# Kernel tuning notes

Measured on AMD Instinct MI355X. Metric: run time of the kernel, lower is better.

## Reference

```python
import jax, jax.numpy as jnp
import numpy as np

B, S, H, I, RH, P, K, NH = 4, 1024, 1024, 4096, 256, 16, 4, 16
TEMP = 1.0


def setup_inputs() -> dict:
    key = jax.random.key(0)
    ks = jax.random.split(key, 10)
    g = lambda k, shape: (jax.random.normal(k, shape, jnp.float32) * 0.02)
    return {
        "hidden_states": jax.random.normal(ks[0], (B, S, H), jnp.float32),
        "ln1_w": jnp.ones((H,), jnp.float32),
        "ln1_b": jnp.zeros((H,), jnp.float32),
        "Wqkv": g(ks[1], (3 * H, H)),
        "bqkv": jnp.zeros((3 * H,), jnp.float32),
        "Wo": g(ks[2], (H, H)),
        "bo": jnp.zeros((H,), jnp.float32),
        "ln2_w": jnp.ones((H,), jnp.float32),
        "ln2_b": jnp.zeros((H,), jnp.float32),
        "Wr1": g(ks[3], (RH, H)),
        "br1": jnp.zeros((RH,), jnp.float32),
        "Wr2": g(ks[4], (P, RH)),
        "br2": jnp.zeros((P,), jnp.float32),
        "W1": g(ks[5], (I, H)),
        "b1": jnp.zeros((I,), jnp.float32),
        "W2": g(ks[6], (H, I)),
        "b2": jnp.zeros((H,), jnp.float32),
    }


def _layernorm(x, w, b, eps=1e-5):
    m = x.mean(-1, keepdims=True)
    v = jnp.mean((x - m) ** 2, axis=-1, keepdims=True)
    return (x - m) * jax.lax.rsqrt(v + eps) * w + b


def _forward(hidden_states, ln1_w, ln1_b, Wqkv, bqkv, Wo, bo,
             ln2_w, ln2_b, Wr1, br1, Wr2, br2, W1, b1, W2, b2):
    Dh = H // NH
    # --- attention sub-block (GPT-2 style causal self-attention) ---
    x = _layernorm(hidden_states, ln1_w, ln1_b)
    qkv = x @ Wqkv.T + bqkv                                  # [B,S,3H]
    q, k, v = jnp.split(qkv, 3, axis=-1)
    split = lambda t: t.reshape(B, S, NH, Dh).transpose(0, 2, 1, 3)  # [B,NH,S,Dh]
    q, k, v = split(q), split(k), split(v)
    scores = jnp.einsum('bhqd,bhkd->bhqk', q, k) * (1.0 / np.float32(np.sqrt(Dh)))
    causal = jnp.tril(jnp.ones((S, S), bool))
    scores = jnp.where(causal, scores, jnp.float32(-1e9))
    attn = jax.nn.softmax(scores, axis=-1)
    ctx = jnp.einsum('bhqk,bhkd->bhqd', attn, v)
    ctx = ctx.transpose(0, 2, 1, 3).reshape(B, S, H)
    h = hidden_states + ctx @ Wo.T + bo                      # residual 1

    # --- routed MLP sub-block ---
    x2 = _layernorm(h, ln2_w, ln2_b)
    # router MLP (eval mode: no dropout)
    r = jax.nn.relu(x2 @ Wr1.T + br1) @ Wr2.T + br2          # [B,S,P]
    probs = jax.nn.softmax(r / TEMP, axis=-1)
    top_vals, top_idx = jax.lax.top_k(probs, K)              # [B,S,K]
    # scatter top-k probs back to pathway axis, then renormalize
    sel = jnp.sum(jax.nn.one_hot(top_idx, P, dtype=probs.dtype) * top_vals[..., None], axis=-2)  # [B,S,P]
    w = sel / (sel.sum(-1, keepdims=True) + 1e-8)

    # block-diagonal pathway MLP: pathway p uses contiguous slices of W1/W2
    Hp, Ip = H // P, I // P
    pidx = jnp.arange(P)
    W1b = W1.reshape(P, Ip, P, Hp)[pidx, :, pidx, :]         # [P,Ip,Hp]
    b1b = b1.reshape(P, Ip)
    W2b = W2.reshape(P, Hp, P, Ip)[pidx, :, pidx, :]         # [P,Hp,Ip]
    b2b = b2.reshape(P, Hp)
    hb = x2.reshape(B, S, P, Hp)
    inter = jax.nn.gelu(jnp.einsum('bsph,pih->bspi', hb, W1b) + b1b)
    po = jnp.einsum('bspi,phi->bsph', inter, W2b) + b2b       # [B,S,P,Hp]
    mlp_out = (po * w[..., None]).reshape(B, S, H)
    return h + mlp_out


def reference(hidden_states, ln1_w, ln1_b, Wqkv, bqkv, Wo, bo,
              ln2_w, ln2_b, Wr1, br1, Wr2, br2, W1, b1, W2, b2):
    return _forward(hidden_states, ln1_w, ln1_b, Wqkv, bqkv, Wo, bo,
                    ln2_w, ln2_b, Wr1, br1, Wr2, br2, W1, b1, W2, b2)
```

## Files before the change

kernel.cpp:

```cpp
#include <hip/hip_runtime.h>


#define USH unsigned short

typedef __attribute__((ext_vector_type(8))) short s16x8;
typedef __attribute__((ext_vector_type(4))) float f32x4;

__device__ __forceinline__ float bf2f(USH u) {
    union { unsigned int i; float f; } x; x.i = ((unsigned int)u) << 16; return x.f;
}
__device__ __forceinline__ USH f2bf(float f) {
    unsigned int x = __float_as_uint(f);
    unsigned int r = (x + 0x7fffu + ((x >> 16) & 1u)) >> 16;
    return (USH)r;
}
__device__ __forceinline__ const USH* pick(const void* raw, const USH* ar, bool bf16in) {
    return bf16in ? (const USH*)raw : ar;
}

__device__ __forceinline__ void async16(const USH* g, USH* lds_base) {
    __builtin_amdgcn_global_load_lds((const __attribute__((address_space(1))) unsigned int*)g,
                                     (__attribute__((address_space(3))) unsigned int*)lds_base,
                                     16, 0, 0);
}

struct CvtArgs {
    const void* src[17];
    unsigned off[18];
};

__global__ __launch_bounds__(256) void convert_kernel(CvtArgs a, USH* __restrict__ arena,
                                                      const unsigned* __restrict__ det)
{
    if (*det != 0x3F800000u) return;
    int s = blockIdx.y + 1;
    unsigned n4 = (a.off[s + 1] - a.off[s]) >> 2;
    ushort4* dst = (ushort4*)(arena + a.off[s]);
    const float4* sf = (const float4*)a.src[s];
    for (unsigned i = blockIdx.x * 256u + threadIdx.x; i < n4; i += gridDim.x * 256u) {
        float4 f = sf[i];
        ushort4 o;
        o.x = f2bf(f.x); o.y = f2bf(f.y); o.z = f2bf(f.z); o.w = f2bf(f.w);
        dst[i] = o;
    }
}

__global__ __launch_bounds__(256) void ln_kernel(const void* __restrict__ in,
                                                 const unsigned* __restrict__ det,
                                                 const void* __restrict__ gwr, const USH* __restrict__ gwa,
                                                 const void* __restrict__ gbr, const USH* __restrict__ gba,
                                                 const unsigned* __restrict__ wdet,
                                                 USH* __restrict__ out)
{
    bool bf16w = (*wdet != 0x3F800000u);
    const USH* gw = pick(gwr, gwa, bf16w);
    const USH* gb = pick(gbr, gba, bf16w);
    int row = blockIdx.x, tid = threadIdx.x;
    bool bf16in = det && (*det != 0x3F800000u);
    float v0, v1, v2, v3;
    if (bf16in) {
        const USH* r = (const USH*)in + (size_t)row * 1024 + tid * 4;
        ushort4 u = *(const ushort4*)r;
        v0 = bf2f(u.x); v1 = bf2f(u.y); v2 = bf2f(u.z); v3 = bf2f(u.w);
    } else {
        const float* r = (const float*)in + (size_t)row * 1024 + tid * 4;
        float4 f = *(const float4*)r;
        v0 = f.x; v1 = f.y; v2 = f.z; v3 = f.w;
    }
    float s = v0 + v1 + v2 + v3;
    float q = v0*v0 + v1*v1 + v2*v2 + v3*v3;
    #pragma unroll
    for (int o = 32; o >= 1; o >>= 1) { s += __shfl_xor(s, o); q += __shfl_xor(q, o); }
    __shared__ float rs[4], rq[4];
    int wid = tid >> 6;
    if ((tid & 63) == 0) { rs[wid] = s; rq[wid] = q; }
    __syncthreads();
    float S = rs[0] + rs[1] + rs[2] + rs[3];
    float Q = rq[0] + rq[1] + rq[2] + rq[3];
    float mean = S * (1.0f / 1024.0f);
    float var  = Q * (1.0f / 1024.0f) - mean * mean;
    float rstd = rsqrtf(var + 1e-5f);
    int c = tid * 4;
    ushort4 wv = *(const ushort4*)(gw + c);
    ushort4 bv = *(const ushort4*)(gb + c);
    ushort4 o4;
    o4.x = f2bf((v0 - mean) * rstd * bf2f(wv.x) + bf2f(bv.x));
    o4.y = f2bf((v1 - mean) * rstd * bf2f(wv.y) + bf2f(bv.y));
    o4.z = f2bf((v2 - mean) * rstd * bf2f(wv.z) + bf2f(bv.z));
    o4.w = f2bf((v3 - mean) * rstd * bf2f(wv.w) + bf2f(bv.w));
    *(ushort4*)(out + (size_t)row * 1024 + c) = o4;
}

template<int RT, int CT>
__global__ __launch_bounds__(256) void gemm_t(
    const USH* __restrict__ A,
    const void* __restrict__ Wraw, const USH* __restrict__ Warena,
    const void* __restrict__ braw, const USH* __restrict__ barena,
    void* __restrict__ Cout, const void* __restrict__ resid,
    int M, int N, int K, int mode, const unsigned* __restrict__ det)
{
    constexpr int BM = 32 * RT, BN = 32 * CT;
    constexpr int NA8 = BM / 8, NC8 = (BM + BN) / 8, NPW = NC8 / 4;
    bool bf16in = (*det != 0x3F800000u);
    const USH* W    = pick(Wraw, Warena, bf16in);
    const USH* bias = pick(braw, barena, bf16in);
    __shared__ __align__(16) USH As[BM * 64];
    __shared__ __align__(16) USH Bs[BN * 64];
    int tid = threadIdx.x;
    int w = tid >> 6, lane = tid & 63, l15 = lane & 15, quad = lane >> 4;
    int wm = (w & 1) * 16 * RT, wn = (w >> 1) * 16 * CT;
    int m0 = blockIdx.x * BM, n0 = blockIdx.y * BN;
    int lr8 = lane >> 3, g = (lane & 7) ^ lr8;
    int sw = l15 & 7;

    const USH* cp[NPW]; USH* lp[NPW];
    #pragma unroll
    for (int i = 0; i < NPW; ++i) {
        int c = w + 4 * i;
        if (c < NA8) { cp[i] = A + (size_t)(m0 + c * 8 + lr8) * K + g * 8;            lp[i] = &As[c * 512]; }
        else         { cp[i] = W + (size_t)(n0 + (c - NA8) * 8 + lr8) * K + g * 8;    lp[i] = &Bs[(c - NA8) * 512]; }
    }
    f32x4 acc[RT][CT] = {};
    for (int k0 = 0; k0 < K; k0 += 64) {
        __syncthreads();
        #pragma unroll
        for (int i = 0; i < NPW; ++i) { async16(cp[i], lp[i]); cp[i] += 64; }
        __syncthreads();
        s16x8 af[RT][2], bfr[CT][2];
        #pragma unroll
        for (int i = 0; i < RT; ++i) {
            int r = wm + 16*i + l15;
            af[i][0] = *(const s16x8*)&As[r * 64 + ((quad       ^ sw) * 8)];
            af[i][1] = *(const s16x8*)&As[r * 64 + (((quad + 4) ^ sw) * 8)];
        }
        #pragma unroll
        for (int j = 0; j < CT; ++j) {
            int r = wn + 16*j + l15;
            bfr[j][0] = *(const s16x8*)&Bs[r * 64 + ((quad       ^ sw) * 8)];
            bfr[j][1] = *(const s16x8*)&Bs[r * 64 + (((quad + 4) ^ sw) * 8)];
        }
        #pragma unroll
        for (int i = 0; i < RT; ++i)
            #pragma unroll
            for (int j = 0; j < CT; ++j) {
                acc[i][j] = __builtin_amdgcn_mfma_f32_16x16x32_bf16(af[i][0], bfr[j][0], acc[i][j], 0, 0, 0);
                acc[i][j] = __builtin_amdgcn_mfma_f32_16x16x32_bf16(af[i][1], bfr[j][1], acc[i][j], 0, 0, 0);
            }
    }
    bool rf32 = !bf16in;
    float bv[CT];
    #pragma unroll
    for (int j = 0; j < CT; ++j) bv[j] = bf2f(bias[n0 + wn + 16*j + l15]);
    #pragma unroll
    for (int i = 0; i < RT; ++i) {
        int mrow = m0 + wm + 16*i + quad * 4;
        #pragma unroll
        for (int j = 0; j < CT; ++j) {
            int n = n0 + wn + 16*j + l15;
            #pragma unroll
            for (int r = 0; r < 4; ++r) {
                int m = mrow + r;
                float val = acc[i][j][r] + bv[j];
                if (mode == 3) val = fmaxf(val, 0.0f);
                if (mode == 2) {
                    size_t idx = (size_t)m * N + n;
                    val += rf32 ? ((const float*)resid)[idx] : bf2f(((const USH*)resid)[idx]);
                }
                if (mode == 1) {
                    int which = n >> 10, head = (n >> 6) & 15, d = n & 63;
                    int b = m >> 10, sdx = m & 1023;
                    ((USH*)Cout)[(((size_t)(which * 64 + b * 16 + head)) * 1024 + sdx) * 64 + d] = f2bf(val);
                } else {
                    ((float*)Cout)[(size_t)m * N + n] = val;
                }
            }
        }
    }
}

__global__ __launch_bounds__(256) void attn_mfma(const USH* __restrict__ qkv,
                                                 USH* __restrict__ ctx)
{
    int bh = blockIdx.x;
    int qb = (gridDim.y - 1) - blockIdx.y;
    int q0 = qb * 64;
    int tid = threadIdx.x, w = tid >> 6, lane = tid & 63, l15 = lane & 15, quad = lane >> 4;
    __shared__ __align__(16) USH Kt[64][72];
    __shared__ __align__(16) USH Vt[80][72];
    __shared__ __align__(16) USH Pb[4][16][72];
    const USH* Qb = qkv + (size_t)bh * 65536;
    const USH* Kb = qkv + (size_t)(64 + bh) * 65536;
    const USH* Vb = qkv + (size_t)(128 + bh) * 65536;
    s16x8 qf[2];
    {
        const USH* qp = Qb + (size_t)(q0 + 16*w + l15) * 64 + quad * 8;
        qf[0] = *(const s16x8*)qp;
        qf[1] = *(const s16x8*)(qp + 32);
    }
    for (int i = tid; i < 16 * 72; i += 256) (&Vt[64][0])[i] = 0x3F80;
    f32x4 oacc[4] = {};
    f32x4 lacc = {};
    int sr = tid & 63, scb = tid >> 6;
    int rowb = 16*w + quad * 4;
    for (int kt = 0; kt <= qb; ++kt) {
        int k0 = kt << 6;
        __syncthreads();
        {
            const USH* kg = Kb + (size_t)(k0 + sr) * 64 + scb * 16;
            uint4 k0v = *(const uint4*)kg;
            uint4 k1v = *(const uint4*)(kg + 8);
            *(uint4*)&Kt[sr][scb * 16]     = k0v;
            *(uint4*)&Kt[sr][scb * 16 + 8] = k1v;
            const USH* vg = Vb + (size_t)(k0 + sr) * 64 + scb * 16;
            uint4 v0v = *(const uint4*)vg;
            uint4 v1v = *(const uint4*)(vg + 8);
            USH tmp[16];
            *(uint4*)tmp       = v0v;
            *(uint4*)(tmp + 8) = v1v;
            #pragma unroll
            for (int i = 0; i < 16; ++i) Vt[scb * 16 + i][sr] = tmp[i];
        }
        __syncthreads();
        f32x4 sacc[4] = {};
        #pragma unroll
        for (int t = 0; t < 4; ++t) {
            s16x8 kf0 = *(const s16x8*)&Kt[16*t + l15][quad * 8];
            s16x8 kf1 = *(const s16x8*)&Kt[16*t + l15][32 + quad * 8];
            sacc[t] = __builtin_amdgcn_mfma_f32_16x16x32_bf16(qf[0], kf0, sacc[t], 0, 0, 0);
            sacc[t] = __builtin_amdgcn_mfma_f32_16x16x32_bf16(qf[1], kf1, sacc[t], 0, 0, 0);
        }
        bool diag = (kt == qb);
        #pragma unroll
        for (int t = 0; t < 4; ++t)
            #pragma unroll
            for (int r = 0; r < 4; ++r) {
                bool masked = diag && (16*t + l15 > rowb + r);
                float pv = masked ? 0.0f : __expf(sacc[t][r] * 0.125f);
                Pb[w][quad*4 + r][16*t + l15] = f2bf(pv);
            }
        s16x8 pf0 = *(const s16x8*)&Pb[w][l15][quad * 8];
        s16x8 pf1 = *(const s16x8*)&Pb[w][l15][32 + quad * 8];
        #pragma unroll
        for (int t = 0; t < 4; ++t) {
            s16x8 vf0 = *(const s16x8*)&Vt[16*t + l15][quad * 8];
            s16x8 vf1 = *(const s16x8*)&Vt[16*t + l15][32 + quad * 8];
            oacc[t] = __builtin_amdgcn_mfma_f32_16x16x32_bf16(pf0, vf0, oacc[t], 0, 0, 0);
            oacc[t] = __builtin_amdgcn_mfma_f32_16x16x32_bf16(pf1, vf1, oacc[t], 0, 0, 0);
        }
        s16x8 of0 = *(const s16x8*)&Vt[64 + l15][quad * 8];
        s16x8 of1 = *(const s16x8*)&Vt[64 + l15][32 + quad * 8];
        lacc = __builtin_amdgcn_mfma_f32_16x16x32_bf16(pf0, of0, lacc, 0, 0, 0);
        lacc = __builtin_amdgcn_mfma_f32_16x16x32_bf16(pf1, of1, lacc, 0, 0, 0);
    }
    int b = bh >> 4, hh = bh & 15;
    float inv[4];
    #pragma unroll
    for (int r = 0; r < 4; ++r) inv[r] = 1.0f / lacc[r];
    #pragma unroll
    for (int t = 0; t < 4; ++t)
        #pragma unroll
        for (int r = 0; r < 4; ++r) {
            int q = q0 + 16*w + quad * 4 + r;
            int d = 16*t + l15;
            ctx[((size_t)(b * 1024 + q)) * 1024 + hh * 64 + d] = f2bf(oacc[t][r] * inv[r]);
        }
}

__global__ __launch_bounds__(64) void router_kernel(const float* __restrict__ r1,
                                                    const void* __restrict__ Wr2raw, const USH* __restrict__ Wr2a,
                                                    const void* __restrict__ br2raw, const USH* __restrict__ br2a,
                                                    const unsigned* __restrict__ det,
                                                    float* __restrict__ wout)
{
    bool bf16in = (*det != 0x3F800000u);
    const USH* Wr2 = pick(Wr2raw, Wr2a, bf16in);
    const USH* br2 = pick(br2raw, br2a, bf16in);
    int tok = blockIdx.x, lane = threadIdx.x;
    int p = lane & 15, c = lane >> 4;
    const float* row = r1 + (size_t)tok * 256;
    const USH* wr = Wr2 + p * 256 + c * 64;
    float s = 0.0f;
    #pragma unroll
    for (int i = 0; i < 64; i += 4) {
        ushort4 u = *(const ushort4*)(wr + i);
        s = fmaf(bf2f(u.x), row[c*64 + i + 0], s);
        s = fmaf(bf2f(u.y), row[c*64 + i + 1], s);
        s = fmaf(bf2f(u.z), row[c*64 + i + 2], s);
        s = fmaf(bf2f(u.w), row[c*64 + i + 3], s);
    }
    s += __shfl_xor(s, 16);
    s += __shfl_xor(s, 32);
    s += bf2f(br2[p]);
    float mx = s;
    #pragma unroll
    for (int o = 8; o >= 1; o >>= 1) mx = fmaxf(mx, __shfl_xor(mx, o));
    float e = __expf(s - mx);
    float sum = e;
    #pragma unroll
    for (int o = 8; o >= 1; o >>= 1) sum += __shfl_xor(sum, o);
    float prob = e / sum;
    int rank = 0;
    int base = lane & 48;
    #pragma unroll
    for (int j = 0; j < 16; ++j) {
        float pj = __shfl(prob, base + j);
        rank += (pj > prob) || (pj == prob && j < p);
    }
    float sel = (rank < 4) ? prob : 0.0f;
    float ssum = sel;
    #pragma unroll
    for (int o = 8; o >= 1; o >>= 1) ssum += __shfl_xor(ssum, o);
    float wv = sel / (ssum + 1e-8f);
    if (lane < 16) wout[(size_t)tok * 16 + lane] = wv;
}

__global__ __launch_bounds__(256) void pw1_kernel(
    const USH* __restrict__ x2,
    const void* __restrict__ W1raw, const USH* __restrict__ W1a,
    const void* __restrict__ b1raw, const USH* __restrict__ b1a,
    USH* __restrict__ inter, const unsigned* __restrict__ det)
{
    bool bf16in = (*det != 0x3F800000u);
    const USH* W1 = pick(W1raw, W1a, bf16in);
    const USH* b1 = pick(b1raw, b1a, bf16in);
    int p = blockIdx.z;
    __shared__ __align__(16) USH As[64 * 64];
    __shared__ __align__(16) USH Bs[128 * 64];
    int tid = threadIdx.x;
    int w = tid >> 6, lane = tid & 63, l15 = lane & 15, quad = lane >> 4;
    int wm = (w & 1) * 32, wn = (w >> 1) * 64;
    int m0 = blockIdx.x * 64, n0 = blockIdx.y * 128;
    int lr8 = lane >> 3, g = (lane & 7) ^ lr8;
    int sw = l15 & 7;

    #pragma unroll
    for (int i = 0; i < 6; ++i) {
        int c = w + 4 * i;
        if (c < 8) async16(x2 + (size_t)(m0 + c * 8 + lr8) * 1024 + p * 64 + g * 8, &As[c * 512]);
        else       async16(W1 + (size_t)(p * 256 + n0 + (c - 8) * 8 + lr8) * 1024 + p * 64 + g * 8, &Bs[(c - 8) * 512]);
    }
    __syncthreads();
    f32x4 acc[2][4] = {};
    s16x8 af[2][2], bfr[4][2];
    #pragma unroll
    for (int i = 0; i < 2; ++i) {
        int r = wm + 16*i + l15;
        af[i][0] = *(const s16x8*)&As[r * 64 + ((quad       ^ sw) * 8)];
        af[i][1] = *(const s16x8*)&As[r * 64 + (((quad + 4) ^ sw) * 8)];
    }
    #pragma unroll
    for (int j = 0; j < 4; ++j) {
        int r = wn + 16*j + l15;
        bfr[j][0] = *(const s16x8*)&Bs[r * 64 + ((quad       ^ sw) * 8)];
        bfr[j][1] = *(const s16x8*)&Bs[r * 64 + (((quad + 4) ^ sw) * 8)];
    }
    #pragma unroll
    for (int i = 0; i < 2; ++i)
        #pragma unroll
        for (int j = 0; j < 4; ++j) {
            acc[i][j] = __builtin_amdgcn_mfma_f32_16x16x32_bf16(af[i][0], bfr[j][0], acc[i][j], 0, 0, 0);
            acc[i][j] = __builtin_amdgcn_mfma_f32_16x16x32_bf16(af[i][1], bfr[j][1], acc[i][j], 0, 0, 0);
        }
    #pragma unroll
    for (int j = 0; j < 4; ++j) {
        int n = n0 + wn + 16*j + l15;
        float bias1 = bf2f(b1[p * 256 + n]);
        #pragma unroll
        for (int i = 0; i < 2; ++i) {
            int mrow = m0 + wm + 16*i + quad * 4;
            #pragma unroll
            for (int r = 0; r < 4; ++r) {
                float s = acc[i][j][r] + bias1;
                float u = 0.7978845608028654f * (s + 0.044715f * s * s * s);
                float e = __expf(2.0f * u);
                float gl = s * (1.0f - 1.0f / (e + 1.0f));
                inter[((size_t)p * 4096 + mrow + r) * 256 + n] = f2bf(gl);
            }
        }
    }
}

__global__ __launch_bounds__(256) void pw2_kernel(
    const USH* __restrict__ inter, const float* __restrict__ hbuf,
    const float* __restrict__ wbuf,
    const void* __restrict__ W2raw, const USH* __restrict__ W2a,
    const void* __restrict__ b2raw, const USH* __restrict__ b2a,
    void* __restrict__ out, const unsigned* __restrict__ det)
{
    bool bf16in = (*det != 0x3F800000u);
    const USH* W2 = pick(W2raw, W2a, bf16in);
    const USH* b2 = pick(b2raw, b2a, bf16in);
    int p = blockIdx.y;
    __shared__ __align__(16) USH As[64 * 64];
    __shared__ __align__(16) USH Bs[64 * 64];
    int tid = threadIdx.x;
    int w = tid >> 6, lane = tid & 63, l15 = lane & 15, quad = lane >> 4;
    int wm = (w & 1) * 32, wn = (w >> 1) * 32;
    int m0 = blockIdx.x * 64;
    int lr8 = lane >> 3, g = (lane & 7) ^ lr8;
    int sw = l15 & 7;

    const USH* cp[4]; USH* lp[4];
    #pragma unroll
    for (int i = 0; i < 4; ++i) {
        int c = w + 4 * i;
        if (c < 8) { cp[i] = inter + ((size_t)p * 4096 + m0 + c * 8 + lr8) * 256 + g * 8; lp[i] = &As[c * 512]; }
        else       { cp[i] = W2 + (size_t)(p * 64 + (c - 8) * 8 + lr8) * 4096 + p * 256 + g * 8; lp[i] = &Bs[(c - 8) * 512]; }
    }
    f32x4 acc[2][2] = {};
    #pragma unroll
    for (int ks = 0; ks < 4; ++ks) {
        __syncthreads();
        #pragma unroll
        for (int i = 0; i < 4; ++i) { async16(cp[i], lp[i]); cp[i] += 64; }
        __syncthreads();
        s16x8 af[2][2], bfr[2][2];
        #pragma unroll
        for (int i = 0; i < 2; ++i) {
            int r = wm + 16*i + l15;
            af[i][0] = *(const s16x8*)&As[r * 64 + ((quad       ^ sw) * 8)];
            af[i][1] = *(const s16x8*)&As[r * 64 + (((quad + 4) ^ sw) * 8)];
        }
        #pragma unroll
        for (int j = 0; j < 2; ++j) {
            int r = wn + 16*j + l15;
            bfr[j][0] = *(const s16x8*)&Bs[r * 64 + ((quad       ^ sw) * 8)];
            bfr[j][1] = *(const s16x8*)&Bs[r * 64 + (((quad + 4) ^ sw) * 8)];
        }
        #pragma unroll
        for (int i = 0; i < 2; ++i)
            #pragma unroll
            for (int j = 0; j < 2; ++j) {
                acc[i][j] = __builtin_amdgcn_mfma_f32_16x16x32_bf16(af[i][0], bfr[j][0], acc[i][j], 0, 0, 0);
                acc[i][j] = __builtin_amdgcn_mfma_f32_16x16x32_bf16(af[i][1], bfr[j][1], acc[i][j], 0, 0, 0);
            }
    }
    bool f32out = !bf16in;
    #pragma unroll
    for (int i = 0; i < 2; ++i) {
        int tok0 = m0 + wm + 16*i + quad * 4;
        float wp[4];
        #pragma unroll
        for (int r = 0; r < 4; ++r) wp[r] = wbuf[(size_t)(tok0 + r) * 16 + p];
        #pragma unroll
        for (int j = 0; j < 2; ++j) {
            int hl = wn + 16*j + l15;
            int hcol = p * 64 + hl;
            float bias2 = bf2f(b2[p * 64 + hl]);
            #pragma unroll
            for (int r = 0; r < 4; ++r) {
                size_t o = (size_t)(tok0 + r) * 1024 + hcol;
                float val = hbuf[o] + (acc[i][j][r] + bias2) * wp[r];
                if (f32out) ((float*)out)[o] = val;
                else        ((USH*)out)[o]   = f2bf(val);
            }
        }
    }
}

extern "C" void kernel_launch(void* const* d_in, const int* in_sizes, int n_in,
                              void* d_out, int out_size, void* d_ws, size_t ws_size,
                              hipStream_t stream) {
    (void)n_in; (void)out_size; (void)ws_size;
    const unsigned* det = (const unsigned*)d_in[1];

    CvtArgs ca;
    unsigned off = 0;
    for (int i = 0; i < 17; ++i) { ca.src[i] = d_in[i]; ca.off[i] = off; off += (unsigned)in_sizes[i]; }
    ca.off[17] = off;

    USH* arena = (USH*)d_ws;
    const USH* ln1w_a = arena + ca.off[1];
    const USH* ln1b_a = arena + ca.off[2];
    const USH* Wqkv_a = arena + ca.off[3];
    const USH* bqkv_a = arena + ca.off[4];
    const USH* Wo_a   = arena + ca.off[5];
    const USH* bo_a   = arena + ca.off[6];
    const USH* ln2w_a = arena + ca.off[7];
    const USH* ln2b_a = arena + ca.off[8];
    const USH* Wr1_a  = arena + ca.off[9];
    const USH* br1_a  = arena + ca.off[10];
    const USH* Wr2_a  = arena + ca.off[11];
    const USH* br2_a  = arena + ca.off[12];
    const USH* W1_a   = arena + ca.off[13];
    const USH* b1_a   = arena + ca.off[14];
    const USH* W2_a   = arena + ca.off[15];
    const USH* b2_a   = arena + ca.off[16];

    size_t arenaB = ((size_t)off * 2 + 255) & ~(size_t)255;
    char* base = (char*)d_ws;
    USH*   x     = (USH*)(base + arenaB);
    USH*   qkvt  = (USH*)(base + arenaB + 8388608);
    float* h     = (float*)(base + arenaB + 8388608 + 25165824);
    USH*   x2    = (USH*)(base + arenaB + 8388608 + 25165824 + 16777216);
    float* r1    = (float*)qkvt;
    float* wbuf  = (float*)(base + arenaB + 8388608 + 25165824 + 16777216 + 8388608);
    USH*   inter = x;
    USH*   ctx   = x;

    convert_kernel<<<dim3(256, 16), 256, 0, stream>>>(ca, arena, det);
    ln_kernel<<<4096, 256, 0, stream>>>(d_in[0], det, d_in[1], ln1w_a, d_in[2], ln1b_a, det, x);
    gemm_t<4,4><<<dim3(32, 24), 256, 0, stream>>>(x, d_in[3], Wqkv_a, d_in[4], bqkv_a, qkvt, nullptr, 4096, 3072, 1024, 1, det);
    attn_mfma<<<dim3(64, 16), 256, 0, stream>>>(qkvt, ctx);
    gemm_t<4,4><<<dim3(32, 8), 256, 0, stream>>>(ctx, d_in[5], Wo_a, d_in[6], bo_a, h, d_in[0], 4096, 1024, 1024, 2, det);
    ln_kernel<<<4096, 256, 0, stream>>>(h, nullptr, d_in[7], ln2w_a, d_in[8], ln2b_a, det, x2);
    gemm_t<2,2><<<dim3(64, 4), 256, 0, stream>>>(x2, d_in[9], Wr1_a, d_in[10], br1_a, r1, nullptr, 4096, 256, 1024, 3, det);
    router_kernel<<<4096, 64, 0, stream>>>(r1, d_in[11], Wr2_a, d_in[12], br2_a, det, wbuf);
    pw1_kernel<<<dim3(64, 2, 16), 256, 0, stream>>>(x2, d_in[13], W1_a, d_in[14], b1_a, inter, det);
    pw2_kernel<<<dim3(64, 16), 256, 0, stream>>>(inter, h, wbuf, d_in[15], W2_a, d_in[16], b2_a, d_out, det);
}
```

Baseline: 298.7 us.

## Fuse pathway MLP up/down projections into one kernel and shrink GEMM tiles

Merges the two pathway MLP kernels into a single kernel. Each block computes the GELU intermediate for 64 tokens and all 256 intermediate columns and keeps it in LDS (64KB, swizzled), then runs the down-projection from LDS. This removes the global write and read of the bf16 intermediate and one launch, but uses more LDS per block and more accumulator registers, which may reduce occupancy. The Wo and router GEMMs also switch to smaller tile templates with larger grids, to get more blocks onto the CUs.

Measured after the change: 285.0 us. 1.05x faster.

```diff
diff --git a/kernel.cpp b/kernel.cpp
--- a/kernel.cpp
+++ b/kernel.cpp
@@ -314,143 +314,136 @@
     if (lane < 16) wout[(size_t)tok * 16 + lane] = wv;
 }
 
-__global__ __launch_bounds__(256) void pw1_kernel(
+__global__ __launch_bounds__(256) void pw_fused(
     const USH* __restrict__ x2,
     const void* __restrict__ W1raw, const USH* __restrict__ W1a,
     const void* __restrict__ b1raw, const USH* __restrict__ b1a,
-    USH* __restrict__ inter, const unsigned* __restrict__ det)
+    const void* __restrict__ W2raw, const USH* __restrict__ W2a,
+    const void* __restrict__ b2raw, const USH* __restrict__ b2a,
+    const float* __restrict__ hbuf, const float* __restrict__ wbuf,
+    void* __restrict__ out, const unsigned* __restrict__ det)
 {
     bool bf16in = (*det != 0x3F800000u);
     const USH* W1 = pick(W1raw, W1a, bf16in);
     const USH* b1 = pick(b1raw, b1a, bf16in);
-    int p = blockIdx.z;
-    __shared__ __align__(16) USH As[64 * 64];
-    __shared__ __align__(16) USH Bs[128 * 64];
-    int tid = threadIdx.x;
-    int w = tid >> 6, lane = tid & 63, l15 = lane & 15, quad = lane >> 4;
-    int wm = (w & 1) * 32, wn = (w >> 1) * 64;
-    int m0 = blockIdx.x * 64, n0 = blockIdx.y * 128;
-    int lr8 = lane >> 3, g = (lane & 7) ^ lr8;
-    int sw = l15 & 7;
-
-    #pragma unroll
-    for (int i = 0; i < 6; ++i) {
-        int c = w + 4 * i;
-        if (c < 8) async16(x2 + (size_t)(m0 + c * 8 + lr8) * 1024 + p * 64 + g * 8, &As[c * 512]);
-        else       async16(W1 + (size_t)(p * 256 + n0 + (c - 8) * 8 + lr8) * 1024 + p * 64 + g * 8, &Bs[(c - 8) * 512]);
-    }
-    __syncthreads();
-    f32x4 acc[2][4] = {};
-    s16x8 af[2][2], bfr[4][2];
-    #pragma unroll
-    for (int i = 0; i < 2; ++i) {
-        int r = wm + 16*i + l15;
-        af[i][0] = *(const s16x8*)&As[r * 64 + ((quad       ^ sw) * 8)];
-        af[i][1] = *(const s16x8*)&As[r * 64 + (((quad + 4) ^ sw) * 8)];
-    }
-    #pragma unroll
-    for (int j = 0; j < 4; ++j) {
-        int r = wn + 16*j + l15;
-        bfr[j][0] = *(const s16x8*)&Bs[r * 64 + ((quad       ^ sw) * 8)];
-        bfr[j][1] = *(const s16x8*)&Bs[r * 64 + (((quad + 4) ^ sw) * 8)];
-    }
-    #pragma unroll
-    for (int i = 0; i < 2; ++i)
-        #pragma unroll
-        for (int j = 0; j < 4; ++j) {
-            acc[i][j] = __builtin_amdgcn_mfma_f32_16x16x32_bf16(af[i][0], bfr[j][0], acc[i][j], 0, 0, 0);
-            acc[i][j] = __builtin_amdgcn_mfma_f32_16x16x32_bf16(af[i][1], bfr[j][1], acc[i][j], 0, 0, 0);
-        }
-    #pragma unroll
-    for (int j = 0; j < 4; ++j) {
-        int n = n0 + wn + 16*j + l15;
-        float bias1 = bf2f(b1[p * 256 + n]);
-        #pragma unroll
-        for (int i = 0; i < 2; ++i) {
-            int mrow = m0 + wm + 16*i + quad * 4;
-            #pragma unroll
-            for (int r = 0; r < 4; ++r) {
-                float s = acc[i][j][r] + bias1;
-                float u = 0.7978845608028654f * (s + 0.044715f * s * s * s);
-                float e = __expf(2.0f * u);
-                float gl = s * (1.0f - 1.0f / (e + 1.0f));
-                inter[((size_t)p * 4096 + mrow + r) * 256 + n] = f2bf(gl);
-            }
-        }
-    }
-}
-
-__global__ __launch_bounds__(256) void pw2_kernel(
-    const USH* __restrict__ inter, const float* __restrict__ hbuf,
-    const float* __restrict__ wbuf,
-    const void* __restrict__ W2raw, const USH* __restrict__ W2a,
-    const void* __restrict__ b2raw, const USH* __restrict__ b2a,
-    void* __restrict__ out, const unsigned* __restrict__ det)
-{
-    bool bf16in = (*det != 0x3F800000u);
     const USH* W2 = pick(W2raw, W2a, bf16in);
     const USH* b2 = pick(b2raw, b2a, bf16in);
     int p = blockIdx.y;
-    __shared__ __align__(16) USH As[64 * 64];
-    __shared__ __align__(16) USH Bs[64 * 64];
+    int m0 = blockIdx.x * 64;
+    __shared__ __align__(16) USH lds[32768];
+    USH* As  = lds;
+    USH* Bs1 = lds + 4096;
+    USH* Is  = lds;
+    USH* Bs2 = lds + 16384;
     int tid = threadIdx.x;
     int w = tid >> 6, lane = tid & 63, l15 = lane & 15, quad = lane >> 4;
-    int wm = (w & 1) * 32, wn = (w >> 1) * 32;
-    int m0 = blockIdx.x * 64;
     int lr8 = lane >> 3, g = (lane & 7) ^ lr8;
     int sw = l15 & 7;
 
-    const USH* cp[4]; USH* lp[4];
-    #pragma unroll
-    for (int i = 0; i < 4; ++i) {
+    #pragma unroll
+    for (int i = 0; i < 10; ++i) {
         int c = w + 4 * i;
-        if (c < 8) { cp[i] = inter + ((size_t)p * 4096 + m0 + c * 8 + lr8) * 256 + g * 8; lp[i] = &As[c * 512]; }
-        else       { cp[i] = W2 + (size_t)(p * 64 + (c - 8) * 8 + lr8) * 4096 + p * 256 + g * 8; lp[i] = &Bs[(c - 8) * 512]; }
-    }
-    f32x4 acc[2][2] = {};
-    #pragma unroll
-    for (int ks = 0; ks < 4; ++ks) {
-        __syncthreads();
-        #pragma unroll
-        for (int i = 0; i < 4; ++i) { async16(cp[i], lp[i]); cp[i] += 64; }
-        __syncthreads();
-        s16x8 af[2][2], bfr[2][2];
+        if (c < 8) async16(x2 + (size_t)(m0 + c * 8 + lr8) * 1024 + p * 64 + g * 8, &As[c * 512]);
+        else       async16(W1 + (size_t)(p * 256 + (c - 8) * 8 + lr8) * 1024 + p * 64 + g * 8, &Bs1[(c - 8) * 512]);
+    }
+    __syncthreads();
+
+    int wmA = (w & 1) * 32, wnA = (w >> 1) * 128;
+    f32x4 accA[2][8] = {};
+    {
+        s16x8 af[2][2];
         #pragma unroll
         for (int i = 0; i < 2; ++i) {
-            int r = wm + 16*i + l15;
+            int r = wmA + 16*i + l15;
             af[i][0] = *(const s16x8*)&As[r * 64 + ((quad       ^ sw) * 8)];
             af[i][1] = *(const s16x8*)&As[r * 64 + (((quad + 4) ^ sw) * 8)];
         }
         #pragma unroll
+        for (int j = 0; j < 8; ++j) {
+            int r = wnA + 16*j + l15;
+            s16x8 b0 = *(const s16x8*)&Bs1[r * 64 + ((quad       ^ sw) * 8)];
+            s16x8 b1f = *(const s16x8*)&Bs1[r * 64 + (((quad + 4) ^ sw) * 8)];
+            #pragma unroll
+            for (int i = 0; i < 2; ++i) {
+                accA[i][j] = __builtin_amdgcn_mfma_f32_16x16x32_bf16(af[i][0], b0,  accA[i][j], 0, 0, 0);
+                accA[i][j] = __builtin_amdgcn_mfma_f32_16x16x32_bf16(af[i][1], b1f, accA[i][j], 0, 0, 0);
+            }
+        }
+    }
+    __syncthreads();
+
+    #pragma unroll
+    for (int ks = 0; ks < 4; ++ks)
+        #pragma unroll
+        for (int i = 0; i < 2; ++i) {
+            int c = w + 4 * i;
+            async16(W2 + (size_t)(p * 64 + c * 8 + lr8) * 4096 + p * 256 + ks * 64 + g * 8,
+                    &Bs2[ks * 4096 + c * 512]);
+        }
+
+    #pragma unroll
+    for (int j = 0; j < 8; ++j) {
+        int n1 = wnA + 16*j + l15;
+        float bias1 = bf2f(b1[p * 256 + n1]);
+        int slab = n1 >> 6, cs = (n1 >> 3) & 7, e = n1 & 7;
+        #pragma unroll
+        for (int i = 0; i < 2; ++i) {
+            int mb = wmA + 16*i + quad * 4;
+            #pragma unroll
+            for (int r = 0; r < 4; ++r) {
+                int m = mb + r;
+                float s = accA[i][j][r] + bias1;
+                float u = 0.7978845608028654f * (s + 0.044715f * s * s * s);
+                float eu = __expf(2.0f * u);
+                float gl = s * (1.0f - 1.0f / (eu + 1.0f));
+                Is[slab * 4096 + m * 64 + ((cs ^ (m & 7)) * 8) + e] = f2bf(gl);
+            }
+        }
+    }
+    __syncthreads();
+
+    int wmB = (w & 1) * 32, wnB = (w >> 1) * 32;
+    f32x4 accB[2][2] = {};
+    #pragma unroll
+    for (int ks = 0; ks < 4; ++ks) {
+        s16x8 af[2][2], bfr[2][2];
+        #pragma unroll
+        for (int i = 0; i < 2; ++i) {
+            int r = wmB + 16*i + l15;
+            af[i][0] = *(const s16x8*)&Is[ks * 4096 + r * 64 + ((quad       ^ sw) * 8)];
+            af[i][1] = *(const s16x8*)&Is[ks * 4096 + r * 64 + (((quad + 4) ^ sw) * 8)];
+        }
+        #pragma unroll
         for (int j = 0; j < 2; ++j) {
-            int r = wn + 16*j + l15;
-            bfr[j][0] = *(const s16x8*)&Bs[r * 64 + ((quad       ^ sw) * 8)];
-            bfr[j][1] = *(const s16x8*)&Bs[r * 64 + (((quad + 4) ^ sw) * 8)];
+            int r = wnB + 16*j + l15;
+            bfr[j][0] = *(const s16x8*)&Bs2[ks * 4096 + r * 64 + ((quad       ^ sw) * 8)];
+            bfr[j][1] = *(const s16x8*)&Bs2[ks * 4096 + r * 64 + (((quad + 4) ^ sw) * 8)];
         }
         #pragma unroll
         for (int i = 0; i < 2; ++i)
             #pragma unroll
             for (int j = 0; j < 2; ++j) {
-                acc[i][j] = __builtin_amdgcn_mfma_f32_16x16x32_bf16(af[i][0], bfr[j][0], acc[i][j], 0, 0, 0);
-                acc[i][j] = __builtin_amdgcn_mfma_f32_16x16x32_bf16(af[i][1], bfr[j][1], acc[i][j], 0, 0, 0);
-            }
-    }
+                accB[i][j] = __builtin_amdgcn_mfma_f32_16x16x32_bf16(af[i][0], bfr[j][0], accB[i][j], 0, 0, 0);
+                accB[i][j] = __builtin_amdgcn_mfma_f32_16x16x32_bf16(af[i][1], bfr[j][1], accB[i][j], 0, 0, 0);
+            }
+    }
+
     bool f32out = !bf16in;
     #pragma unroll
     for (int i = 0; i < 2; ++i) {
-        int tok0 = m0 + wm + 16*i + quad * 4;
+        int tok0 = m0 + wmB + 16*i + quad * 4;
         float wp[4];
         #pragma unroll
         for (int r = 0; r < 4; ++r) wp[r] = wbuf[(size_t)(tok0 + r) * 16 + p];
         #pragma unroll
         for (int j = 0; j < 2; ++j) {
-            int hl = wn + 16*j + l15;
+            int hl = wnB + 16*j + l15;
             int hcol = p * 64 + hl;
             float bias2 = bf2f(b2[p * 64 + hl]);
             #pragma unroll
             for (int r = 0; r < 4; ++r) {
                 size_t o = (size_t)(tok0 + r) * 1024 + hcol;
-                float val = hbuf[o] + (acc[i][j][r] + bias2) * wp[r];
+                float val = hbuf[o] + (accB[i][j][r] + bias2) * wp[r];
                 if (f32out) ((float*)out)[o] = val;
                 else        ((USH*)out)[o]   = f2bf(val);
             }
@@ -495,17 +488,17 @@
     USH*   x2    = (USH*)(base + arenaB + 8388608 + 25165824 + 16777216);
     float* r1    = (float*)qkvt;
     float* wbuf  = (float*)(base + arenaB + 8388608 + 25165824 + 16777216 + 8388608);
-    USH*   inter = x;
     USH*   ctx   = x;
 
     convert_kernel<<<dim3(256, 16), 256, 0, stream>>>(ca, arena, det);
     ln_kernel<<<4096, 256, 0, stream>>>(d_in[0], det, d_in[1], ln1w_a, d_in[2], ln1b_a, det, x);
     gemm_t<4,4><<<dim3(32, 24), 256, 0, stream>>>(x, d_in[3], Wqkv_a, d_in[4], bqkv_a, qkvt, nullptr, 4096, 3072, 1024, 1, det);
     attn_mfma<<<dim3(64, 16), 256, 0, stream>>>(qkvt, ctx);
-    gemm_t<4,4><<<dim3(32, 8), 256, 0, stream>>>(ctx, d_in[5], Wo_a, d_in[6], bo_a, h, d_in[0], 4096, 1024, 1024, 2, det);
+    gemm_t<2,4><<<dim3(64, 8), 256, 0, stream>>>(ctx, d_in[5], Wo_a, d_in[6], bo_a, h, d_in[0], 4096, 1024, 1024, 2, det);
     ln_kernel<<<4096, 256, 0, stream>>>(h, nullptr, d_in[7], ln2w_a, d_in[8], ln2b_a, det, x2);
-    gemm_t<2,2><<<dim3(64, 4), 256, 0, stream>>>(x2, d_in[9], Wr1_a, d_in[10], br1_a, r1, nullptr, 4096, 256, 1024, 3, det);
+    gemm_t<1,2><<<dim3(128, 4), 256, 0, stream>>>(x2, d_in[9], Wr1_a, d_in[10], br1_a, r1, nullptr, 4096, 256, 1024, 3, det);
     router_kernel<<<4096, 64, 0, stream>>>(r1, d_in[11], Wr2_a, d_in[12], br2_a, det, wbuf);
-    pw1_kernel<<<dim3(64, 2, 16), 256, 0, stream>>>(x2, d_in[13], W1_a, d_in[14], b1_a, inter, det);
-    pw2_kernel<<<dim3(64, 16), 256, 0, stream>>>(inter, h, wbuf, d_in[15], W2_a, d_in[16], b2_a, d_out, det);
-}
+    pw_fused<<<dim3(64, 16), 256, 0, stream>>>(x2, d_in[13], W1_a, d_in[14], b1_a,
+                                               d_in[15], W2_a, d_in[16], b2_a,
+                                               h, wbuf, d_out, det);
+}
```
